# Kernel optimization log

Measured on AMD Instinct MI355X. Metric: run time of the kernel, lower is better.

## Reference

```python
import jax, jax.numpy as jnp
import numpy as np

N, E, P = 20000, 320000, 100000
TC, HID, H, OUT, PH = 256, 64, 4, 256, 512


def gat_conv(x, src, dst, n, W, a_src, a_dst, b):
    # PyG GATConv (eval, dropout=0): per-head linear, LeakyReLU(0.2) attention,
    # scatter-softmax over incoming edges, scatter-add aggregation, concat heads + bias.
    Hh, C = a_src.shape
    h = (x @ W).reshape(n, Hh, C)
    alpha_src = (h * a_src).sum(-1)  # [N, H]
    alpha_dst = (h * a_dst).sum(-1)  # [N, H]
    e = jax.nn.leaky_relu(alpha_src[src] + alpha_dst[dst], 0.2)  # [E, H]
    emax = jax.ops.segment_max(e, dst, num_segments=n)
    emax = jnp.where(jnp.isfinite(emax), emax, 0.0)
    p = jnp.exp(e - emax[dst])
    denom = jax.ops.segment_sum(p, dst, num_segments=n)
    alpha = p / jnp.maximum(denom[dst], 1e-16)  # [E, H]
    out = jax.ops.segment_sum(h[src] * alpha[:, :, None], dst, num_segments=n)  # [N, H, C]
    return out.reshape(n, Hh * C) + b


def setup_inputs() -> dict:
    key = jax.random.key(0)
    ks = jax.random.split(key, 24)
    s = 0.05
    inp = {
        "x": jax.random.normal(ks[0], (N, TC), jnp.float32),
        "edge_index": jax.random.randint(ks[1], (2, E), 0, N, jnp.int64),
        "u_nodes": jax.random.randint(ks[2], (P,), 0, N, jnp.int64),
        "v_nodes": jax.random.randint(ks[3], (P,), 0, N, jnp.int64),
        # GATConv 1: in=TC, out=HID per head, heads=H, concat
        "W1": jax.random.normal(ks[4], (TC, H * HID), jnp.float32) * s,
        "a1s": jax.random.normal(ks[5], (H, HID), jnp.float32) * s,
        "a1d": jax.random.normal(ks[6], (H, HID), jnp.float32) * s,
        "b1": jax.random.normal(ks[7], (H * HID,), jnp.float32) * s,
        # GATConv 2: in=H*HID, out=OUT, heads=1
        "W2": jax.random.normal(ks[8], (H * HID, OUT), jnp.float32) * s,
        "a2s": jax.random.normal(ks[9], (1, OUT), jnp.float32) * s,
        "a2d": jax.random.normal(ks[10], (1, OUT), jnp.float32) * s,
        "b2": jax.random.normal(ks[11], (OUT,), jnp.float32) * s,
        # gate MLP: (TC+OUT) -> (TC+OUT)//2 -> 1, Sigmoid
        "gw1": jax.random.normal(ks[12], (TC + OUT, (TC + OUT) // 2), jnp.float32) * s,
        "gb1": jax.random.normal(ks[13], ((TC + OUT) // 2,), jnp.float32) * s,
        "gw2": jax.random.normal(ks[14], ((TC + OUT) // 2, 1), jnp.float32) * s,
        "gb2": jax.random.normal(ks[15], (1,), jnp.float32) * s,
        # predictor: 2*OUT -> PH -> 1 (dropout is identity in eval)
        "pw1": jax.random.normal(ks[16], (2 * OUT, PH), jnp.float32) * s,
        "pb1": jax.random.normal(ks[17], (PH,), jnp.float32) * s,
        "pw2": jax.random.normal(ks[18], (PH, 1), jnp.float32) * s,
        "pb2": jax.random.normal(ks[19], (1,), jnp.float32) * s,
    }
    return inp


def reference(x, edge_index, u_nodes, v_nodes, W1, a1s, a1d, b1, W2, a2s, a2d, b2,
              gw1, gb1, gw2, gb2, pw1, pb1, pw2, pb2):
    n = x.shape[0]
    loops = jnp.arange(n, dtype=edge_index.dtype)
    src = jnp.concatenate([edge_index[0], loops])  # PyG GATConv adds self-loops
    dst = jnp.concatenate([edge_index[1], loops])
    h = jax.nn.elu(gat_conv(x, src, dst, n, W1, a1s, a1d, b1))
    h_graph = gat_conv(h, src, dst, n, W2, a2s, a2d, b2)
    gate_in = jnp.concatenate([x, h_graph], axis=-1)
    g = jax.nn.sigmoid(jax.nn.relu(gate_in @ gw1 + gb1) @ gw2 + gb2)  # [N,1]
    h_final = (1.0 - g) * x + g * h_graph
    pair = jnp.concatenate([h_final[u_nodes], h_final[v_nodes]], axis=-1)  # [P, 2*OUT]
    out = jax.nn.relu(pair @ pw1 + pb1) @ pw2 + pb2
    return out.squeeze(-1)
```

## Files before the change

kernel.cpp:

```cpp
#include <hip/hip_runtime.h>
#include <math.h>

#define N_NODES 20000
#define N_EDGES 320000
#define EPRIME  (N_EDGES + N_NODES)
#define NP      100000

typedef __bf16 bf16x8 __attribute__((ext_vector_type(8)));
typedef float  f32x4  __attribute__((ext_vector_type(4)));

__device__ __forceinline__ float b2f(unsigned short u) {
    union { float f; unsigned int v; } x; x.v = ((unsigned int)u) << 16; return x.f;
}
__device__ __forceinline__ unsigned short f2b(float f) {
    union { float f; unsigned int v; } x; x.f = f;
    unsigned int r = (x.v + 0x7fffu + ((x.v >> 16) & 1u)) >> 16;
    return (unsigned short)r;
}
__device__ __forceinline__ float lrelu02(float v) { return v > 0.0f ? v : 0.2f * v; }

__device__ __forceinline__ void gload16(const void* g, void* l) {
    __builtin_amdgcn_global_load_lds(
        (const __attribute__((address_space(1))) void*)g,
        (__attribute__((address_space(3))) void*)l, 16, 0, 0);
}

template<int BM, int ASRC, int EPI>
__global__ __launch_bounds__(256) void mgemm_k(
    const unsigned short* __restrict__ A0, const unsigned short* __restrict__ A1,
    const unsigned short* __restrict__ BT,
    const float* __restrict__ bias, const float* __restrict__ w2,
    unsigned short* __restrict__ Cb, float* __restrict__ outp,
    float* __restrict__ outp2,
    int M, int K, int Nn)
{
    constexpr int NJA   = BM / 64;
    constexpr int MF    = BM / 32;
    constexpr int WROWS = BM / 2;

    __shared__ unsigned short As[2][BM * 32];
    __shared__ unsigned short Bs[2][4096];

    const int tid = threadIdx.x;
    const int wave = tid >> 6, lane = tid & 63;
    const int row0 = blockIdx.x * BM, col0 = blockIdx.y * 128;
    const int ksub = (((lane & 3) ^ ((lane >> 3) & 3)) * 8);

    const unsigned short* aL[NJA];
    const unsigned short* aH[NJA];
    const unsigned short* bP[2];
    #pragma unroll
    for (int j = 0; j < NJA; ++j) {
        const int r = j * 64 + wave * 16 + (lane >> 2);
        int ar = row0 + r; if (ar > M - 1) ar = M - 1;
        if (ASRC == 0) { aL[j] = A0 + (long)ar * K;  aH[j] = aL[j]; }
        else           { aL[j] = A0 + (long)ar * 256; aH[j] = A1 + (long)ar * 256; }
    }
    #pragma unroll
    for (int j = 0; j < 2; ++j) {
        const int r = j * 64 + wave * 16 + (lane >> 2);
        bP[j] = BT + (long)(col0 + r) * K;
    }

    const int wm = wave >> 1, wn = wave & 1;
    const int lrow = lane & 15;
    const int lks = ((((lane >> 4) ^ ((lane >> 1) & 3)) & 3) * 8);

    f32x4 acc[MF][4] = {};

    const int nT = K >> 5;
    int buf = 0;

    auto stage = [&](int bi, int t) {
        const int k0 = t << 5;
        #pragma unroll
        for (int j = 0; j < NJA; ++j) {
            const unsigned short* ga;
            if (ASRC == 0) ga = aL[j] + k0 + ksub;
            else ga = (k0 < 256) ? (aL[j] + k0 + ksub) : (aH[j] + (k0 - 256) + ksub);
            const int ci = j * 256 + wave * 64 + lane;
            gload16(ga, &As[bi][ci * 8]);
        }
        #pragma unroll
        for (int j = 0; j < 2; ++j) {
            const int ci = j * 256 + wave * 64 + lane;
            gload16(bP[j] + k0 + ksub, &Bs[bi][ci * 8]);
        }
    };

    stage(0, 0);
    __syncthreads();
    for (int t = 0; t < nT; ++t) {
        if (t + 1 < nT) stage(buf ^ 1, t + 1);
        bf16x8 a[MF], b[4];
        #pragma unroll
        for (int i = 0; i < MF; ++i)
            a[i] = *(const bf16x8*)&As[buf][(wm * WROWS + i * 16 + lrow) * 32 + lks];
        #pragma unroll
        for (int j = 0; j < 4; ++j)
            b[j] = *(const bf16x8*)&Bs[buf][(wn * 64 + j * 16 + lrow) * 32 + lks];
        #pragma unroll
        for (int i = 0; i < MF; ++i)
            #pragma unroll
            for (int j = 0; j < 4; ++j)
                acc[i][j] = __builtin_amdgcn_mfma_f32_16x16x32_bf16(a[i], b[j], acc[i][j], 0, 0, 0);
        __syncthreads();
        buf ^= 1;
    }

    if constexpr (EPI == 0 || EPI == 1 || EPI == 4 || EPI == 5) {
        #pragma unroll
        for (int i = 0; i < MF; ++i) {
            #pragma unroll
            for (int p = 0; p < 4; ++p) {
                const int row = row0 + wm * WROWS + i * 16 + (lane >> 4) * 4 + p;
                if (row < M) {
                    #pragma unroll
                    for (int j = 0; j < 4; ++j) {
                        const int col = col0 + wn * 64 + j * 16 + (lane & 15);
                        float v = acc[i][j][p];
                        if (EPI == 1) { v += bias[col]; v = v > 0.f ? v : 0.f; }
                        Cb[(long)row * Nn + col] = f2b(v);
                    }
                }
            }
        }
    }
    if constexpr (EPI == 4 || EPI == 5) {
        #pragma unroll
        for (int i = 0; i < MF; ++i) {
            #pragma unroll
            for (int p = 0; p < 4; ++p) {
                float ps = 0.f, pd = 0.f;
                #pragma unroll
                for (int j = 0; j < 4; ++j) {
                    const int col = col0 + wn * 64 + j * 16 + lrow;
                    ps = fmaf(acc[i][j][p], bias[col], ps);
                    pd = fmaf(acc[i][j][p], w2[col], pd);
                }
                #pragma unroll
                for (int off = 1; off < 16; off <<= 1) {
                    ps += __shfl_xor(ps, off);
                    pd += __shfl_xor(pd, off);
                }
                const int row = row0 + wm * WROWS + i * 16 + (lane >> 4) * 4 + p;
                if (lrow == 0 && row < M) {
                    if (EPI == 4) {
                        const int head = (col0 >> 6) + wn;
                        outp[row * 4 + head]  = ps;
                        outp2[row * 4 + head] = pd;
                    } else {
                        atomicAdd(outp + row, ps);
                        atomicAdd(outp2 + row, pd);
                    }
                }
            }
        }
    }
    if constexpr (EPI == 2) {
        float s[MF][4];
        #pragma unroll
        for (int i = 0; i < MF; ++i) {
            #pragma unroll
            for (int p = 0; p < 4; ++p) {
                float t = 0.f;
                #pragma unroll
                for (int j = 0; j < 4; ++j) {
                    const int col = col0 + wn * 64 + j * 16 + (lane & 15);
                    float v = acc[i][j][p] + bias[col];
                    v = v > 0.f ? v : 0.f;
                    t += v * w2[col];
                }
                s[i][p] = t;
            }
        }
        #pragma unroll
        for (int off = 1; off < 16; off <<= 1) {
            #pragma unroll
            for (int i = 0; i < MF; ++i)
                #pragma unroll
                for (int p = 0; p < 4; ++p)
                    s[i][p] += __shfl_xor(s[i][p], off);
        }
        if ((lane & 15) == 0) {
            #pragma unroll
            for (int i = 0; i < MF; ++i)
                #pragma unroll
                for (int p = 0; p < 4; ++p) {
                    const int row = row0 + wm * WROWS + i * 16 + (lane >> 4) * 4 + p;
                    if (row < M) atomicAdd(outp + row, s[i][p]);
                }
        }
    }
}

__global__ __launch_bounds__(512) void zgemm_k(
    const unsigned short* __restrict__ A0,
    const unsigned short* __restrict__ BT,
    const float* __restrict__ bias,
    unsigned short* __restrict__ Cb,
    int M)
{
    __shared__ unsigned short lds[24576];

    const int tid = threadIdx.x;
    const int wave = tid >> 6, lane = tid & 63;
    const int row0 = blockIdx.x * 128, col0 = blockIdx.y * 256;
    const int ksub = (((tid & 3) ^ ((tid >> 3) & 3)) * 8);

    const unsigned short* aP;
    {
        int ar = row0 + (tid >> 2); if (ar > M - 1) ar = M - 1;
        aP = A0 + (long)ar * 256;
    }
    const unsigned short* bP[2];
    #pragma unroll
    for (int j = 0; j < 2; ++j)
        bP[j] = BT + (long)(col0 + j * 128 + (tid >> 2)) * 256;

    const int wm = wave >> 2, wn = wave & 3;
    const int lrow = lane & 15, g = lane >> 4;
    const int lks = ((((lane >> 4) ^ ((lane >> 1) & 3)) & 3) * 8);

    f32x4 acc[4][4] = {};
    int buf = 0;

    auto stage = [&](int bi, int t) {
        const int k0 = t << 5;
        gload16(aP + k0 + ksub, &lds[bi * 4096 + tid * 8]);
        #pragma unroll
        for (int j = 0; j < 2; ++j)
            gload16(bP[j] + k0 + ksub, &lds[8192 + bi * 8192 + (j * 512 + tid) * 8]);
    };

    stage(0, 0);
    __syncthreads();
    #pragma unroll
    for (int t = 0; t < 8; ++t) {
        if (t + 1 < 8) stage(buf ^ 1, t + 1);
        const unsigned short* as_b = &lds[buf * 4096];
        const unsigned short* bs_b = &lds[8192 + buf * 8192];
        bf16x8 a[4], b[4];
        #pragma unroll
        for (int i = 0; i < 4; ++i)
            a[i] = *(const bf16x8*)&as_b[(wm * 64 + i * 16 + lrow) * 32 + lks];
        #pragma unroll
        for (int j = 0; j < 4; ++j)
            b[j] = *(const bf16x8*)&bs_b[(wn * 64 + j * 16 + lrow) * 32 + lks];
        #pragma unroll
        for (int i = 0; i < 4; ++i)
            #pragma unroll
            for (int j = 0; j < 4; ++j)
                acc[i][j] = __builtin_amdgcn_mfma_f32_16x16x32_bf16(a[i], b[j], acc[i][j], 0, 0, 0);
        __syncthreads();
        buf ^= 1;
    }

    unsigned short* Cs = lds;
    #pragma unroll
    for (int h = 0; h < 2; ++h) {
        if (wm == h) {
            #pragma unroll
            for (int i = 0; i < 4; ++i)
                #pragma unroll
                for (int j = 0; j < 4; ++j)
                    #pragma unroll
                    for (int p = 0; p < 4; ++p) {
                        const int r = i * 16 + g * 4 + p;
                        const int c = wn * 64 + j * 16 + lrow;
                        float v = acc[i][j][p];
                        const int col = col0 + c;
                        if (col < 512) v += bias[col];
                        Cs[r * 256 + c] = f2b(v);
                    }
        }
        __syncthreads();
        #pragma unroll
        for (int q = 0; q < 4; ++q) {
            const int cq = q * 512 + tid;
            const int r = cq >> 5, ch = cq & 31;
            const int row = row0 + h * 64 + r;
            if (row < M)
                *(ulonglong2*)&Cb[(long)row * 1024 + col0 + ch * 8] =
                    *(const ulonglong2*)&Cs[r * 256 + ch * 8];
        }
        __syncthreads();
    }
}

__global__ __launch_bounds__(256) void pair_k(
    const unsigned short* __restrict__ Z, const int* __restrict__ un,
    const int* __restrict__ vn, const float* __restrict__ pw2,
    const float* __restrict__ pb2, float* __restrict__ out)
{
    const int wv = threadIdx.x >> 6, lane = threadIdx.x & 63;
    const int p = blockIdx.x * 4 + wv;
    if (p >= NP) return;
    const int u = un[p], v = vn[p];
    const int c0 = lane * 8;
    const uint4 zu = *(const uint4*)&Z[(long)u * 1024 + c0];
    const uint4 zv = *(const uint4*)&Z[(long)v * 1024 + 512 + c0];
    const float4 w2a = *(const float4*)&pw2[c0];
    const float4 w2b = *(const float4*)&pw2[c0 + 4];

    float zt[8], zb[8];
    zt[0] = b2f(zu.x & 0xffff); zt[1] = b2f(zu.x >> 16);
    zt[2] = b2f(zu.y & 0xffff); zt[3] = b2f(zu.y >> 16);
    zt[4] = b2f(zu.z & 0xffff); zt[5] = b2f(zu.z >> 16);
    zt[6] = b2f(zu.w & 0xffff); zt[7] = b2f(zu.w >> 16);
    zb[0] = b2f(zv.x & 0xffff); zb[1] = b2f(zv.x >> 16);
    zb[2] = b2f(zv.y & 0xffff); zb[3] = b2f(zv.y >> 16);
    zb[4] = b2f(zv.z & 0xffff); zb[5] = b2f(zv.z >> 16);
    zb[6] = b2f(zv.w & 0xffff); zb[7] = b2f(zv.w >> 16);

    const float ww[8] = {w2a.x, w2a.y, w2a.z, w2a.w, w2b.x, w2b.y, w2b.z, w2b.w};
    float s = 0.f;
    #pragma unroll
    for (int q = 0; q < 8; ++q) {
        float t = zt[q] + zb[q];
        t = t > 0.f ? t : 0.f;
        s = fmaf(t, ww[q], s);
    }
    #pragma unroll
    for (int off = 1; off < 64; off <<= 1) s += __shfl_xor(s, off);
    if (lane == 0) out[p] = s + pb2[0];
}

__global__ __launch_bounds__(256) void prep_k(
    const float* __restrict__ x, unsigned short* __restrict__ xb,
    const float* __restrict__ W1, unsigned short* __restrict__ W1t,
    const float* __restrict__ W2, unsigned short* __restrict__ W2t,
    const float* __restrict__ gw1, unsigned short* __restrict__ gw1t,
    const float* __restrict__ pw1, unsigned short* __restrict__ pw1t2,
    int* __restrict__ deg, float* __restrict__ gacc,
    float* __restrict__ as2v, float* __restrict__ ad2v)
{
    const int bid = blockIdx.x, tid = threadIdx.x;
    if (bid < 5000) {
        const int id = bid * 256 + tid;
        const float4 v = ((const float4*)x)[id];
        ushort4 o;
        o.x = f2b(v.x); o.y = f2b(v.y); o.z = f2b(v.z); o.w = f2b(v.w);
        ((ushort4*)xb)[id] = o;
    } else if (bid < 5256) {
        const int id = (bid - 5000) * 256 + tid;
        W1t[(id & 255) * 256 + (id >> 8)] = f2b(W1[id]);
    } else if (bid < 5512) {
        const int id = (bid - 5256) * 256 + tid;
        W2t[(id & 255) * 256 + (id >> 8)] = f2b(W2[id]);
    } else if (bid < 6024) {
        const int id = (bid - 5512) * 256 + tid;
        gw1t[(id & 255) * 512 + (id >> 8)] = f2b(gw1[id]);
    } else if (bid < 7048) {
        const int id = (bid - 6024) * 256 + tid;
        const int r = id >> 9, c = id & 511;
        const int j = (r < 256) ? c : (512 + c);
        const int k = (r < 256) ? r : (r - 256);
        pw1t2[j * 256 + k] = f2b(pw1[id]);
    } else if (bid < 7127) {
        const int i = (bid - 7048) * 256 + tid;
        if (i < N_NODES) deg[i] = 1;
    } else {
        const int i = (bid - 7127) * 256 + tid;
        if (i < 20000) gacc[i] = 0.f;
        else if (i < 40000) as2v[i - 20000] = 0.f;
        else if (i < 60000) ad2v[i - 40000] = 0.f;
    }
}

__global__ __launch_bounds__(256) void deg_count_k(const int* __restrict__ ei, int* __restrict__ deg)
{
    const int e = blockIdx.x * 256 + threadIdx.x;
    if (e < N_EDGES) atomicAdd(&deg[ei[N_EDGES + e]], 1);
}

__global__ __launch_bounds__(1024) void scan_k(const int* __restrict__ deg,
                                               int* __restrict__ indptr,
                                               int* __restrict__ pos)
{
    __shared__ int sums[1024];
    const int tid = threadIdx.x;
    const int CH = 20;
    const int start = tid * CH;
    const int end = min(start + CH, N_NODES);
    int s = 0;
    for (int i = start; i < end; ++i) s += deg[i];
    sums[tid] = s;
    __syncthreads();
    for (int off = 1; off < 1024; off <<= 1) {
        const int v = sums[tid];
        const int add = (tid >= off) ? sums[tid - off] : 0;
        __syncthreads();
        sums[tid] = v + add;
        __syncthreads();
    }
    int pre = sums[tid] - s;
    for (int i = start; i < end; ++i) {
        indptr[i] = pre;
        pos[i] = pre;
        pre += deg[i];
    }
    if (tid == 1023) indptr[N_NODES] = sums[1023];
}

__global__ __launch_bounds__(256) void fill_k(const int* __restrict__ ei,
                                              int* __restrict__ pos, int* __restrict__ csr)
{
    const int i = blockIdx.x * 256 + threadIdx.x;
    if (i < N_EDGES) {
        const int s = ei[i], d = ei[N_EDGES + i];
        const int p = atomicAdd(&pos[d], 1);
        csr[p] = s;
    } else if (i < EPRIME) {
        const int n = i - N_EDGES;
        const int p = atomicAdd(&pos[n], 1);
        csr[p] = n;
    }
}

__global__ __launch_bounds__(256) void agg1_k(
    const unsigned short* __restrict__ h1, const float* __restrict__ as1,
    const float* __restrict__ ad1, const int* __restrict__ indptr,
    const int* __restrict__ csr, const float* __restrict__ b1,
    unsigned short* __restrict__ out)
{
    __shared__ int   ssrc[4][64];
    __shared__ float sp[4][64 * 4];
    const int wv = threadIdx.x >> 6, lane = threadIdx.x & 63;
    const int n = blockIdx.x * 4 + wv;
    if (n >= N_NODES) return;

    const int beg = indptr[n], end = indptr[n + 1];
    const float4 ad = ((const float4*)ad1)[n];
    const int c0 = lane * 4;
    const int hd = lane >> 4;

    float acc[4] = {0.f, 0.f, 0.f, 0.f};
    float psum[4] = {0.f, 0.f, 0.f, 0.f};

    for (int base = beg; base < end; base += 64) {
        const int cnt = min(64, end - base);
        if (lane < cnt) {
            const int s = csr[base + lane];
            const float4 av = ((const float4*)as1)[s];
            float4 p;
            p.x = __expf(lrelu02(av.x + ad.x));
            p.y = __expf(lrelu02(av.y + ad.y));
            p.z = __expf(lrelu02(av.z + ad.z));
            p.w = __expf(lrelu02(av.w + ad.w));
            ssrc[wv][lane] = s;
            *(float4*)&sp[wv][lane * 4] = p;
            psum[0] += p.x; psum[1] += p.y; psum[2] += p.z; psum[3] += p.w;
        }
        asm volatile("s_waitcnt lgkmcnt(0)" ::: "memory");
        __builtin_amdgcn_sched_barrier(0);
        for (int e = 0; e < cnt; ++e) {
            const int s = ssrc[wv][e];
            const float w = sp[wv][e * 4 + hd];
            const ushort4 hv = *(const ushort4*)&h1[(long)s * 256 + c0];
            acc[0] = fmaf(w, b2f(hv.x), acc[0]);
            acc[1] = fmaf(w, b2f(hv.y), acc[1]);
            acc[2] = fmaf(w, b2f(hv.z), acc[2]);
            acc[3] = fmaf(w, b2f(hv.w), acc[3]);
        }
        __builtin_amdgcn_sched_barrier(0);
        __builtin_amdgcn_wave_barrier();
    }

    #pragma unroll
    for (int off = 1; off < 64; off <<= 1) {
        #pragma unroll
        for (int h = 0; h < 4; ++h) psum[h] += __shfl_xor(psum[h], off);
    }
    const float invd = 1.0f / psum[hd];

    ushort4 o;
    float v;
    v = acc[0] * invd + b1[c0 + 0]; o.x = f2b(v > 0.f ? v : (__expf(v) - 1.0f));
    v = acc[1] * invd + b1[c0 + 1]; o.y = f2b(v > 0.f ? v : (__expf(v) - 1.0f));
    v = acc[2] * invd + b1[c0 + 2]; o.z = f2b(v > 0.f ? v : (__expf(v) - 1.0f));
    v = acc[3] * invd + b1[c0 + 3]; o.w = f2b(v > 0.f ? v : (__expf(v) - 1.0f));
    *(ushort4*)&out[(long)n * 256 + c0] = o;
}

__global__ __launch_bounds__(256) void agg2_k(
    const unsigned short* __restrict__ h2, const float* __restrict__ as2,
    const float* __restrict__ ad2, const int* __restrict__ indptr,
    const int* __restrict__ csr, const float* __restrict__ b2,
    unsigned short* __restrict__ outb)
{
    __shared__ int   ssrc[4][64];
    __shared__ float sp[4][64];
    const int wv = threadIdx.x >> 6, lane = threadIdx.x & 63;
    const int n = blockIdx.x * 4 + wv;
    if (n >= N_NODES) return;

    const int beg = indptr[n], end = indptr[n + 1];
    const float adv = ad2[n];
    const int c0 = lane * 4;

    float acc[4] = {0.f, 0.f, 0.f, 0.f};
    float psum = 0.f;

    for (int base = beg; base < end; base += 64) {
        const int cnt = min(64, end - base);
        if (lane < cnt) {
            const int s = csr[base + lane];
            const float p = __expf(lrelu02(as2[s] + adv));
            ssrc[wv][lane] = s;
            sp[wv][lane] = p;
            psum += p;
        }
        asm volatile("s_waitcnt lgkmcnt(0)" ::: "memory");
        __builtin_amdgcn_sched_barrier(0);
        for (int e = 0; e < cnt; ++e) {
            const int s = ssrc[wv][e];
            const float w = sp[wv][e];
            const ushort4 hv = *(const ushort4*)&h2[(long)s * 256 + c0];
            acc[0] = fmaf(w, b2f(hv.x), acc[0]);
            acc[1] = fmaf(w, b2f(hv.y), acc[1]);
            acc[2] = fmaf(w, b2f(hv.z), acc[2]);
            acc[3] = fmaf(w, b2f(hv.w), acc[3]);
        }
        __builtin_amdgcn_sched_barrier(0);
        __builtin_amdgcn_wave_barrier();
    }

    #pragma unroll
    for (int off = 1; off < 64; off <<= 1) psum += __shfl_xor(psum, off);
    const float invd = 1.0f / psum;

    ushort4 o;
    o.x = f2b(acc[0] * invd + b2[c0 + 0]);
    o.y = f2b(acc[1] * invd + b2[c0 + 1]);
    o.z = f2b(acc[2] * invd + b2[c0 + 2]);
    o.w = f2b(acc[3] * invd + b2[c0 + 3]);
    *(ushort4*)&outb[(long)n * 256 + c0] = o;
}

__global__ __launch_bounds__(256) void gatefin2_k(
    const float* __restrict__ gacc, const float* __restrict__ gb2,
    const float* __restrict__ x, const unsigned short* __restrict__ hgb,
    unsigned short* __restrict__ hfb)
{
    const int wid = threadIdx.x >> 6;
    const int lane = threadIdx.x & 63;
    const int n = blockIdx.x * 4 + wid;
    if (n >= N_NODES) return;
    const float g = 1.0f / (1.0f + __expf(-(gacc[n] + gb2[0])));
    #pragma unroll
    for (int q = 0; q < 4; ++q) {
        const int c = q * 64 + lane;
        const float xv = x[(long)n * 256 + c];
        const float hv = b2f(hgb[(long)n * 256 + c]);
        hfb[(long)n * 256 + c] = f2b((1.0f - g) * xv + g * hv);
    }
}

extern "C" void kernel_launch(void* const* d_in, const int* in_sizes, int n_in,
                              void* d_out, int out_size, void* d_ws, size_t ws_size,
                              hipStream_t stream)
{
    const float* x   = (const float*)d_in[0];
    const int*   ei  = (const int*)d_in[1];
    const int*   un  = (const int*)d_in[2];
    const int*   vn  = (const int*)d_in[3];
    const float* W1  = (const float*)d_in[4];
    const float* a1s = (const float*)d_in[5];
    const float* a1d = (const float*)d_in[6];
    const float* b1  = (const float*)d_in[7];
    const float* W2  = (const float*)d_in[8];
    const float* a2s = (const float*)d_in[9];
    const float* a2d = (const float*)d_in[10];
    const float* b2  = (const float*)d_in[11];
    const float* gw1 = (const float*)d_in[12];
    const float* gb1 = (const float*)d_in[13];
    const float* gw2 = (const float*)d_in[14];
    const float* gb2 = (const float*)d_in[15];
    const float* pw1 = (const float*)d_in[16];
    const float* pb1 = (const float*)d_in[17];
    const float* pw2 = (const float*)d_in[18];
    const float* pb2 = (const float*)d_in[19];
    float* out = (float*)d_out;

    dim3 b256(256);

    if (ws_size < 58720256u) return;

    unsigned short* Z     = (unsigned short*)d_ws;
    unsigned short* bufHb = Z;
    unsigned short* hgb   = Z + 5120000;
    unsigned short* xb    = Z + 10240000;
    unsigned short* hfb   = Z + 20480000;
    unsigned short* W1t   = hfb + 5120000;
    unsigned short* W2t   = W1t + 65536;
    unsigned short* gw1t  = W2t + 65536;
    unsigned short* pw1t2 = gw1t + 131072;
    float* as1v = (float*)(pw1t2 + 262144);
    float* ad1v = as1v + 80000;
    float* as2v = ad1v + 80000;
    float* ad2v = as2v + 20000;
    int* deg    = (int*)(ad2v + 20000);
    int* indptr = deg + 20000;
    int* pos    = indptr + 20032;
    int* csr    = pos + 20000;
    float* gacc = (float*)(csr + EPRIME);

    prep_k<<<7362, b256, 0, stream>>>(x, xb, W1, W1t, W2, W2t, gw1, gw1t,
                                      pw1, pw1t2, deg, gacc, as2v, ad2v);
    deg_count_k<<<(N_EDGES + 255) / 256, b256, 0, stream>>>(ei, deg);
    scan_k<<<1, 1024, 0, stream>>>(deg, indptr, pos);
    fill_k<<<(EPRIME + 255) / 256, b256, 0, stream>>>(ei, pos, csr);

    mgemm_k<64, 0, 4><<<dim3(313, 2), b256, 0, stream>>>(
        xb, nullptr, W1t, a1s, a1d, bufHb, as1v, ad1v, N_NODES, 256, 256);
    agg1_k<<<5000, b256, 0, stream>>>(bufHb, as1v, ad1v, indptr, csr, b1, hfb);

    mgemm_k<64, 0, 5><<<dim3(313, 2), b256, 0, stream>>>(
        hfb, nullptr, W2t, a2s, a2d, bufHb, as2v, ad2v, N_NODES, 256, 256);
    agg2_k<<<5000, b256, 0, stream>>>(bufHb, as2v, ad2v, indptr, csr, b2, hgb);

    mgemm_k<64, 1, 2><<<dim3(313, 2), b256, 0, stream>>>(
        xb, hgb, gw1t, gb1, gw2, nullptr, gacc, nullptr, N_NODES, 512, 256);
    gatefin2_k<<<5000, b256, 0, stream>>>(gacc, gb2, x, hgb, hfb);

    zgemm_k<<<dim3(157, 4), dim3(512), 0, stream>>>(hfb, pw1t2, pb1, Z, N_NODES);

    pair_k<<<25000, b256, 0, stream>>>(Z, un, vn, pw2, pb2, out);
}
```

Before: 237.2 us.

## Triple-buffer GEMM LDS staging with counted vmcnt waits and one barrier

Both MFMA GEMM kernels move from double to triple LDS buffering. Global-to-LDS loads are now issued two stages ahead, and each iteration waits on a counted vmcnt before a single s_barrier instead of a full __syncthreads after compute. The goal is to overlap more memory latency with MFMA work and cut barrier stalls. In exchange LDS use grows, which may lower occupancy, and mgemm_k is now restricted to BM=64 by a static_assert.

```diff
diff --git a/kernel.cpp b/kernel.cpp
--- a/kernel.cpp
+++ b/kernel.cpp
@@ -37,24 +37,24 @@
     constexpr int NJA   = BM / 64;
     constexpr int MF    = BM / 32;
     constexpr int WROWS = BM / 2;
-
-    __shared__ unsigned short As[2][BM * 32];
-    __shared__ unsigned short Bs[2][4096];
+    static_assert(NJA == 1, "counted vmcnt assumes 3 loads/stage (BM=64)");
+
+    __shared__ unsigned short As[3][BM * 32];
+    __shared__ unsigned short Bs[3][4096];
 
     const int tid = threadIdx.x;
     const int wave = tid >> 6, lane = tid & 63;
     const int row0 = blockIdx.x * BM, col0 = blockIdx.y * 128;
     const int ksub = (((lane & 3) ^ ((lane >> 3) & 3)) * 8);
 
-    const unsigned short* aL[NJA];
-    const unsigned short* aH[NJA];
+    const unsigned short* aL;
+    const unsigned short* aH;
     const unsigned short* bP[2];
-    #pragma unroll
-    for (int j = 0; j < NJA; ++j) {
-        const int r = j * 64 + wave * 16 + (lane >> 2);
+    {
+        const int r = wave * 16 + (lane >> 2);
         int ar = row0 + r; if (ar > M - 1) ar = M - 1;
-        if (ASRC == 0) { aL[j] = A0 + (long)ar * K;  aH[j] = aL[j]; }
-        else           { aL[j] = A0 + (long)ar * 256; aH[j] = A1 + (long)ar * 256; }
+        if (ASRC == 0) { aL = A0 + (long)ar * K;  aH = aL; }
+        else           { aL = A0 + (long)ar * 256; aH = A1 + (long)ar * 256; }
     }
     #pragma unroll
     for (int j = 0; j < 2; ++j) {
@@ -69,29 +69,28 @@
     f32x4 acc[MF][4] = {};
 
     const int nT = K >> 5;
-    int buf = 0;
 
     auto stage = [&](int bi, int t) {
         const int k0 = t << 5;
-        #pragma unroll
-        for (int j = 0; j < NJA; ++j) {
-            const unsigned short* ga;
-            if (ASRC == 0) ga = aL[j] + k0 + ksub;
-            else ga = (k0 < 256) ? (aL[j] + k0 + ksub) : (aH[j] + (k0 - 256) + ksub);
-            const int ci = j * 256 + wave * 64 + lane;
-            gload16(ga, &As[bi][ci * 8]);
-        }
-        #pragma unroll
-        for (int j = 0; j < 2; ++j) {
-            const int ci = j * 256 + wave * 64 + lane;
-            gload16(bP[j] + k0 + ksub, &Bs[bi][ci * 8]);
-        }
+        const unsigned short* ga;
+        if (ASRC == 0) ga = aL + k0 + ksub;
+        else ga = (k0 < 256) ? (aL + k0 + ksub) : (aH + (k0 - 256) + ksub);
+        gload16(ga, &As[bi][(wave * 64 + lane) * 8]);
+        #pragma unroll
+        for (int j = 0; j < 2; ++j)
+            gload16(bP[j] + k0 + ksub, &Bs[bi][(j * 256 + wave * 64 + lane) * 8]);
     };
 
     stage(0, 0);
-    __syncthreads();
+    stage(1, 1);
     for (int t = 0; t < nT; ++t) {
-        if (t + 1 < nT) stage(buf ^ 1, t + 1);
+        if (t >= nT - 1) { asm volatile("s_waitcnt vmcnt(0)" ::: "memory"); }
+        else             { asm volatile("s_waitcnt vmcnt(3)" ::: "memory"); }
+        __builtin_amdgcn_sched_barrier(0);
+        __builtin_amdgcn_s_barrier();
+        __builtin_amdgcn_sched_barrier(0);
+        if (t + 2 < nT) stage((t + 2) % 3, t + 2);
+        const int buf = t % 3;
         bf16x8 a[MF], b[4];
         #pragma unroll
         for (int i = 0; i < MF; ++i)
@@ -99,13 +98,13 @@
         #pragma unroll
         for (int j = 0; j < 4; ++j)
             b[j] = *(const bf16x8*)&Bs[buf][(wn * 64 + j * 16 + lrow) * 32 + lks];
+        asm volatile("s_waitcnt lgkmcnt(0)" ::: "memory");
+        __builtin_amdgcn_sched_barrier(0);
         #pragma unroll
         for (int i = 0; i < MF; ++i)
             #pragma unroll
             for (int j = 0; j < 4; ++j)
                 acc[i][j] = __builtin_amdgcn_mfma_f32_16x16x32_bf16(a[i], b[j], acc[i][j], 0, 0, 0);
-        __syncthreads();
-        buf ^= 1;
     }
 
     if constexpr (EPI == 0 || EPI == 1 || EPI == 4 || EPI == 5) {
@@ -201,7 +200,7 @@
     unsigned short* __restrict__ Cb,
     int M)
 {
-    __shared__ unsigned short lds[24576];
+    __shared__ unsigned short lds[36864];
 
     const int tid = threadIdx.x;
     const int wave = tid >> 6, lane = tid & 63;
@@ -223,23 +222,27 @@
     const int lks = ((((lane >> 4) ^ ((lane >> 1) & 3)) & 3) * 8);
 
     f32x4 acc[4][4] = {};
-    int buf = 0;
 
     auto stage = [&](int bi, int t) {
         const int k0 = t << 5;
         gload16(aP + k0 + ksub, &lds[bi * 4096 + tid * 8]);
         #pragma unroll
         for (int j = 0; j < 2; ++j)
-            gload16(bP[j] + k0 + ksub, &lds[8192 + bi * 8192 + (j * 512 + tid) * 8]);
+            gload16(bP[j] + k0 + ksub, &lds[12288 + bi * 8192 + (j * 512 + tid) * 8]);
     };
 
     stage(0, 0);
-    __syncthreads();
+    stage(1, 1);
     #pragma unroll
     for (int t = 0; t < 8; ++t) {
-        if (t + 1 < 8) stage(buf ^ 1, t + 1);
-        const unsigned short* as_b = &lds[buf * 4096];
-        const unsigned short* bs_b = &lds[8192 + buf * 8192];
+        if (t >= 7) { asm volatile("s_waitcnt vmcnt(0)" ::: "memory"); }
+        else        { asm volatile("s_waitcnt vmcnt(3)" ::: "memory"); }
+        __builtin_amdgcn_sched_barrier(0);
+        __builtin_amdgcn_s_barrier();
+        __builtin_amdgcn_sched_barrier(0);
+        if (t + 2 < 8) stage((t + 2) % 3, t + 2);
+        const unsigned short* as_b = &lds[(t % 3) * 4096];
+        const unsigned short* bs_b = &lds[12288 + (t % 3) * 8192];
         bf16x8 a[4], b[4];
         #pragma unroll
         for (int i = 0; i < 4; ++i)
@@ -247,14 +250,15 @@
         #pragma unroll
         for (int j = 0; j < 4; ++j)
             b[j] = *(const bf16x8*)&bs_b[(wn * 64 + j * 16 + lrow) * 32 + lks];
+        asm volatile("s_waitcnt lgkmcnt(0)" ::: "memory");
+        __builtin_amdgcn_sched_barrier(0);
         #pragma unroll
         for (int i = 0; i < 4; ++i)
             #pragma unroll
             for (int j = 0; j < 4; ++j)
                 acc[i][j] = __builtin_amdgcn_mfma_f32_16x16x32_bf16(a[i], b[j], acc[i][j], 0, 0, 0);
-        __syncthreads();
-        buf ^= 1;
-    }
+    }
+    __syncthreads();
 
     unsigned short* Cs = lds;
     #pragma unroll
```

Result: no change. 236.5 us (-0.3%).
